# Optimization experiments

Hardware: AMD Instinct MI355X
Metric: run time of the kernel (lower is better)

The kernel has to match this reference:

```python
import jax, jax.numpy as jnp
import numpy as np

B, S, E = 2, 2048, 256
H, D = 8, 32
INF = 2.0 ** 15
EPS = 1e-5


def setup_inputs() -> dict:
    key = jax.random.key(0)
    ks = jax.random.split(key, 10)
    x = jax.random.normal(ks[0], (B, S, E), dtype=jnp.float32)
    mask = jax.random.uniform(ks[1], (B, S), dtype=jnp.float32)
    attn_bias = jax.random.normal(ks[2], (B, H, S, S), dtype=jnp.float32)
    # torch Linear weights have shape (out_dim, in_dim)
    sc = 1.0 / np.sqrt(E)
    Wq = jax.random.normal(ks[3], (H * D, E), dtype=jnp.float32) * sc
    Wk = jax.random.normal(ks[4], (H * D, E), dtype=jnp.float32) * sc
    Wv = jax.random.normal(ks[5], (H * D, E), dtype=jnp.float32) * sc
    # gating init: W=0, b=1 -> perturb slightly so grads are non-trivial
    Wg = jax.random.normal(ks[6], (H * D, E), dtype=jnp.float32) * 0.02
    bg = jnp.ones((H * D,), dtype=jnp.float32)
    # final init: zeros -> perturb slightly
    Wo = jax.random.normal(ks[7], (E, H * D), dtype=jnp.float32) * 0.02
    bo = jnp.zeros((E,), dtype=jnp.float32)
    return {"x": x, "mask": mask, "attn_bias": attn_bias,
            "Wq": Wq, "Wk": Wk, "Wv": Wv, "Wg": Wg, "bg": bg,
            "Wo": Wo, "bo": bo}


def _split_heads(t):
    # [B, S, H*D] -> [B, H, S, D]
    b, s, _ = t.shape
    return t.reshape(b, s, H, D).transpose(0, 2, 1, 3)


def reference(x, mask, attn_bias, Wq, Wk, Wv, Wg, bg, Wo, bo):
    # LayerNorm without affine params
    mu = jnp.mean(x, axis=-1, keepdims=True)
    var = jnp.var(x, axis=-1, keepdims=True)
    xn = (x - mu) * jax.lax.rsqrt(var + EPS)

    scale = 1.0 / jnp.sqrt(jnp.asarray(D, dtype=x.dtype))
    q = _split_heads(xn @ Wq.T) * scale          # [B,H,S,D]
    k = _split_heads(xn @ Wk.T)                   # [B,H,S,D]
    v = _split_heads(xn @ Wv.T)                   # [B,H,S,D]
    gate = jax.nn.sigmoid(_split_heads(xn @ Wg.T + bg))  # [B,H,S,D]

    logits = jnp.einsum('bhic,bhjc->bhij', q, k) + attn_bias  # [B,H,S,S]
    logits = jnp.where(mask[:, None, None, :] < 0.5, -INF, logits)
    attn = jax.nn.softmax(logits, axis=-1)

    out = gate * jnp.einsum('bhij,bhjc->bhic', attn, v)  # [B,H,S,D]
    out = out.transpose(0, 2, 1, 3).reshape(x.shape[0], x.shape[1], H * D)
    return out @ Wo.T + bo
```

## Files before the change

### kernel.cpp

```cpp
#include <hip/hip_runtime.h>
#include <stdint.h>

typedef unsigned short u16;
typedef unsigned int   u32;
typedef __attribute__((ext_vector_type(8))) short    short8;
typedef __attribute__((ext_vector_type(8))) _Float16 half8;
typedef __attribute__((ext_vector_type(4))) _Float16 half4;
typedef __attribute__((ext_vector_type(4))) float    f32x4;

#define BB 2
#define SS 2048
#define EE 256
#define HH 8
#define DDh 32

__device__ __forceinline__ u16 f2b(float f){
  union{u32 u; float f;} c; c.f = f;
  u32 r = c.u + 0x7fffu + ((c.u >> 16) & 1u);
  return (u16)(r >> 16);
}
__device__ __forceinline__ u32 pack2(float lo, float hi){
  return (u32)f2b(lo) | ((u32)f2b(hi) << 16);
}

__device__ __forceinline__ float blockSum(float v, float* red){
  #pragma unroll
  for (int off = 32; off > 0; off >>= 1) v += __shfl_xor(v, off, 64);
  int w = threadIdx.x >> 6;
  if ((threadIdx.x & 63) == 0) red[w] = v;
  __syncthreads();
  float r = (red[0] + red[1]) + (red[2] + red[3]);
  __syncthreads();
  return r;
}

__global__ __launch_bounds__(256) void k_cvt(const float* __restrict__ Wq,
    const float* __restrict__ Wk, const float* __restrict__ Wv,
    const float* __restrict__ Wg, const float* __restrict__ Wo,
    _Float16* __restrict__ wcat, _Float16* __restrict__ woh){
  int id = blockIdx.x * 256 + threadIdx.x;
  int g = id >> 14, idx = id & 16383;
  const float* srcs[5] = {Wq, Wk, Wv, Wg, Wo};
  float4 v = ((const float4*)srcs[g])[idx];
  half4 h = {(_Float16)v.x, (_Float16)v.y, (_Float16)v.z, (_Float16)v.w};
  _Float16* dst = (g < 4) ? (wcat + (size_t)g * 65536) : woh;
  *(half4*)(dst + (size_t)idx * 4) = h;
}

__global__ __launch_bounds__(256) void k_ln(const float* __restrict__ x,
                                            _Float16* __restrict__ xnh){
  __shared__ float red[4];
  int row = blockIdx.x, t = threadIdx.x;
  float xv = x[(size_t)row * EE + t];
  float s  = blockSum(xv, red);
  float ss = blockSum(xv * xv, red);
  float mean = s * (1.0f / EE);
  float var  = ss * (1.0f / EE) - mean * mean;
  float rstd = rsqrtf(var + 1e-5f);
  xnh[(size_t)row * EE + t] = (_Float16)((xv - mean) * rstd);
}

__global__ __launch_bounds__(256) void k_proj(const _Float16* __restrict__ xnh,
    const _Float16* __restrict__ wcat, const float* __restrict__ bg,
    u16* __restrict__ qws, u16* __restrict__ kws,
    u16* __restrict__ vtws, float* __restrict__ gws){
  int t = threadIdx.x, wave = t >> 6, lane = t & 63;
  int q4 = lane >> 4, ln = lane & 15;
  int Mblk = blockIdx.x >> 4, Nblk = blockIdx.x & 15;
  int m0 = Mblk * 64, n0 = Nblk * 64 + wave * 16;
  int n = n0 + ln;
  const _Float16* brow = wcat + (size_t)n * EE;
  f32x4 acc[4];
  #pragma unroll
  for (int mb = 0; mb < 4; ++mb) acc[mb] = (f32x4){0.f,0.f,0.f,0.f};
  for (int k0 = 0; k0 < EE; k0 += 32){
    half8 bf = *(const half8*)(brow + k0 + q4 * 8);
    #pragma unroll
    for (int mb = 0; mb < 4; ++mb){
      half8 af = *(const half8*)(xnh + (size_t)(m0 + mb * 16 + ln) * EE + k0 + q4 * 8);
      acc[mb] = __builtin_amdgcn_mfma_f32_16x16x32_f16(af, bf, acc[mb], 0, 0, 0);
    }
  }
  int mat = n >> 8, c = n & 255;
  int h = c >> 5, d = c & 31;
  int b = m0 >> 11, s0 = (m0 & (SS - 1));
  size_t rowbase = ((size_t)b * HH + h) * SS;
  if (mat == 0){
    #pragma unroll
    for (int mb = 0; mb < 4; ++mb)
      #pragma unroll
      for (int r = 0; r < 4; ++r){
        int s = s0 + mb * 16 + q4 * 4 + r;
        qws[(rowbase + s) * DDh + d] = f2b(acc[mb][r] * 0.17677669529663687f);
      }
  } else if (mat == 1){
    #pragma unroll
    for (int mb = 0; mb < 4; ++mb)
      #pragma unroll
      for (int r = 0; r < 4; ++r){
        int s = s0 + mb * 16 + q4 * 4 + r;
        kws[(rowbase + s) * DDh + d] = f2b(acc[mb][r]);
      }
  } else if (mat == 2){
    u16* vrow = vtws + (((size_t)b * HH + h) * DDh + d) * SS;
    #pragma unroll
    for (int mb = 0; mb < 4; ++mb){
      ushort4 pk;
      pk.x = f2b(acc[mb][0]); pk.y = f2b(acc[mb][1]);
      pk.z = f2b(acc[mb][2]); pk.w = f2b(acc[mb][3]);
      *(ushort4*)(vrow + s0 + mb * 16 + q4 * 4) = pk;
    }
  } else {
    float bgv = bg[c];
    #pragma unroll
    for (int mb = 0; mb < 4; ++mb)
      #pragma unroll
      for (int r = 0; r < 4; ++r){
        int s = s0 + mb * 16 + q4 * 4 + r;
        gws[(rowbase + s) * DDh + d] = 1.0f / (1.0f + __expf(-(acc[mb][r] + bgv)));
      }
  }
}

__global__ __launch_bounds__(256) void k_attn(const u16* __restrict__ qws,
    const u16* __restrict__ kws, const u16* __restrict__ vtws,
    const float* __restrict__ gws, const float* __restrict__ bias,
    const float* __restrict__ mask, _Float16* __restrict__ gouth){
  int t = threadIdx.x;
  int wave = t >> 6, lane = t & 63;
  int q4 = lane >> 4, ln = lane & 15;
  int bh = blockIdx.x >> 5;
  int i0 = (blockIdx.x & 31) * 64 + wave * 16;
  int b = bh >> 3, h = bh & 7;

  short8 qf = *(const short8*)(qws + (((size_t)bh * SS + i0 + ln) * DDh) + q4 * 8);

  const u16*  kb   = kws  + (size_t)bh * SS * DDh;
  const u16*  vt   = vtws + (size_t)bh * DDh * SS;
  const float* br  = bias + ((size_t)bh * SS + i0) * SS;
  const float* mrow= mask + (size_t)b * SS;

  f32x4 O0 = {0.f,0.f,0.f,0.f}, O1 = {0.f,0.f,0.f,0.f};
  float m_run = -INFINITY, l_run = 0.0f;
  const f32x4 zero = {0.f,0.f,0.f,0.f};

  for (int j0 = 0; j0 < SS; j0 += 32){
    short8 ka0 = *(const short8*)(kb + (size_t)(j0 + ln)      * DDh + q4 * 8);
    short8 ka1 = *(const short8*)(kb + (size_t)(j0 + 16 + ln) * DDh + q4 * 8);
    short8 va0 = *(const short8*)(vt + (size_t)ln        * SS + j0 + q4 * 8);
    short8 va1 = *(const short8*)(vt + (size_t)(16 + ln) * SS + j0 + q4 * 8);
    float4 bv0 = *(const float4*)(br + (size_t)ln * SS + j0 + q4 * 4);
    float4 bv1 = *(const float4*)(br + (size_t)ln * SS + j0 + 16 + q4 * 4);
    float4 mv0 = *(const float4*)(mrow + j0 + q4 * 4);
    float4 mv1 = *(const float4*)(mrow + j0 + 16 + q4 * 4);

    f32x4 s0 = __builtin_amdgcn_mfma_f32_16x16x32_bf16(ka0, qf, zero, 0, 0, 0);
    f32x4 s1 = __builtin_amdgcn_mfma_f32_16x16x32_bf16(ka1, qf, zero, 0, 0, 0);

    float lgv[8];
    lgv[0] = (mv0.x >= 0.5f) ? s0[0] + bv0.x : -32768.0f;
    lgv[1] = (mv0.y >= 0.5f) ? s0[1] + bv0.y : -32768.0f;
    lgv[2] = (mv0.z >= 0.5f) ? s0[2] + bv0.z : -32768.0f;
    lgv[3] = (mv0.w >= 0.5f) ? s0[3] + bv0.w : -32768.0f;
    lgv[4] = (mv1.x >= 0.5f) ? s1[0] + bv1.x : -32768.0f;
    lgv[5] = (mv1.y >= 0.5f) ? s1[1] + bv1.y : -32768.0f;
    lgv[6] = (mv1.z >= 0.5f) ? s1[2] + bv1.z : -32768.0f;
    lgv[7] = (mv1.w >= 0.5f) ? s1[3] + bv1.w : -32768.0f;

    float mt = lgv[0];
    #pragma unroll
    for (int r = 1; r < 8; ++r) mt = fmaxf(mt, lgv[r]);
    mt = fmaxf(mt, __shfl_xor(mt, 16, 64));
    mt = fmaxf(mt, __shfl_xor(mt, 32, 64));
    float m_new = fmaxf(m_run, mt);
    float alpha = __expf(m_run - m_new);
    float p[8], ts = 0.0f;
    #pragma unroll
    for (int r = 0; r < 8; ++r){ p[r] = __expf(lgv[r] - m_new); ts += p[r]; }
    ts += __shfl_xor(ts, 16, 64);
    ts += __shfl_xor(ts, 32, 64);
    l_run = l_run * alpha + ts;
    m_run = m_new;
    #pragma unroll
    for (int e = 0; e < 4; ++e){ O0[e] *= alpha; O1[e] *= alpha; }

    u32 P0 = pack2(p[0], p[1]), P1 = pack2(p[2], p[3]);
    u32 P2 = pack2(p[4], p[5]), P3 = pack2(p[6], p[7]);
    int sl  = (q4 & 1) * 32 + ln;
    int sl2 = sl + 16;
    u32 x0 = __shfl((int)P0, sl,  64), x1 = __shfl((int)P1, sl,  64);
    u32 x2 = __shfl((int)P2, sl,  64), x3 = __shfl((int)P3, sl,  64);
    u32 y0 = __shfl((int)P0, sl2, 64), y1 = __shfl((int)P1, sl2, 64);
    u32 y2 = __shfl((int)P2, sl2, 64), y3 = __shfl((int)P3, sl2, 64);
    bool lo = (q4 < 2);
    u32 bb[4];
    bb[0] = lo ? x0 : x2;  bb[1] = lo ? x1 : x3;
    bb[2] = lo ? y0 : y2;  bb[3] = lo ? y1 : y3;
    short8 pf = *(short8*)bb;

    O0 = __builtin_amdgcn_mfma_f32_16x16x32_bf16(va0, pf, O0, 0, 0, 0);
    O1 = __builtin_amdgcn_mfma_f32_16x16x32_bf16(va1, pf, O1, 0, 0, 0);
  }

  float inv = 1.0f / l_run;
  const float* gr = gws + ((size_t)bh * SS + i0 + ln) * DDh;
  float4 g0 = *(const float4*)(gr + q4 * 4);
  float4 g1 = *(const float4*)(gr + 16 + q4 * 4);
  _Float16* orow = gouth + ((size_t)b * SS + (i0 + ln)) * EE + h * DDh;
  half4 w0, w1;
  w0.x = (_Float16)(O0[0] * inv * g0.x);  w0.y = (_Float16)(O0[1] * inv * g0.y);
  w0.z = (_Float16)(O0[2] * inv * g0.z);  w0.w = (_Float16)(O0[3] * inv * g0.w);
  w1.x = (_Float16)(O1[0] * inv * g1.x);  w1.y = (_Float16)(O1[1] * inv * g1.y);
  w1.z = (_Float16)(O1[2] * inv * g1.z);  w1.w = (_Float16)(O1[3] * inv * g1.w);
  *(half4*)(orow + q4 * 4)      = w0;
  *(half4*)(orow + 16 + q4 * 4) = w1;
}

__global__ __launch_bounds__(256) void k_out(const _Float16* __restrict__ gouth,
    const _Float16* __restrict__ woh, const float* __restrict__ bo,
    float* __restrict__ out){
  int t = threadIdx.x, wave = t >> 6, lane = t & 63;
  int q4 = lane >> 4, ln = lane & 15;
  int Mblk = blockIdx.x >> 2, Nblk = blockIdx.x & 3;
  int m0 = Mblk * 64, n0 = Nblk * 64 + wave * 16;
  int n = n0 + ln;
  const _Float16* brow = woh + (size_t)n * EE;
  f32x4 acc[4];
  #pragma unroll
  for (int mb = 0; mb < 4; ++mb) acc[mb] = (f32x4){0.f,0.f,0.f,0.f};
  for (int k0 = 0; k0 < EE; k0 += 32){
    half8 bf = *(const half8*)(brow + k0 + q4 * 8);
    #pragma unroll
    for (int mb = 0; mb < 4; ++mb){
      half8 af = *(const half8*)(gouth + (size_t)(m0 + mb * 16 + ln) * EE + k0 + q4 * 8);
      acc[mb] = __builtin_amdgcn_mfma_f32_16x16x32_f16(af, bf, acc[mb], 0, 0, 0);
    }
  }
  float bov = bo[n];
  #pragma unroll
  for (int mb = 0; mb < 4; ++mb)
    #pragma unroll
    for (int r = 0; r < 4; ++r){
      int m = m0 + mb * 16 + q4 * 4 + r;
      out[(size_t)m * EE + n] = acc[mb][r] + bov;
    }
}

extern "C" void kernel_launch(void* const* d_in, const int* in_sizes, int n_in,
                              void* d_out, int out_size, void* d_ws, size_t ws_size,
                              hipStream_t stream){
  const float* x    = (const float*)d_in[0];
  const float* mask = (const float*)d_in[1];
  const float* bias = (const float*)d_in[2];
  const float* Wq   = (const float*)d_in[3];
  const float* Wk   = (const float*)d_in[4];
  const float* Wv   = (const float*)d_in[5];
  const float* Wg   = (const float*)d_in[6];
  const float* bg   = (const float*)d_in[7];
  const float* Wo   = (const float*)d_in[8];
  const float* bo   = (const float*)d_in[9];
  float* out = (float*)d_out;

  char* ws = (char*)d_ws;
  _Float16* xnh  = (_Float16*)ws;
  u16*  qws  = (u16*) (ws + (2  << 20));
  u16*  kws  = (u16*) (ws + (4  << 20));
  u16*  vtws = (u16*) (ws + (6  << 20));
  float* gws = (float*)(ws + (8  << 20));
  _Float16* gouth = (_Float16*)(ws + (12 << 20));
  _Float16* wcat  = (_Float16*)(ws + (14 << 20));
  _Float16* woh   = (_Float16*)(ws + (15 << 20));

  hipLaunchKernelGGL(k_cvt,  dim3(320),                dim3(256), 0, stream,
                     Wq, Wk, Wv, Wg, Wo, wcat, woh);
  hipLaunchKernelGGL(k_ln,   dim3(BB * SS),            dim3(256), 0, stream, x, xnh);
  hipLaunchKernelGGL(k_proj, dim3(64 * 16),            dim3(256), 0, stream,
                     xnh, wcat, bg, qws, kws, vtws, gws);
  hipLaunchKernelGGL(k_attn, dim3(BB * HH * (SS / 64)), dim3(256), 0, stream,
                     qws, kws, vtws, gws, bias, mask, gouth);
  hipLaunchKernelGGL(k_out,  dim3(64 * 4),             dim3(256), 0, stream,
                     gouth, woh, bo, out);
}
```

Baseline: 435.8 us.

## Double-buffer attention K/V/bias tiles and merge LayerNorm with weight conversion

The attention loop now processes 64-key tiles, with the next tile's K, V and bias loads issued into registers while the current tile computes. This hides global-memory latency on the bias stream, which dominates traffic. It also raises MFMA priority around the PV products and sets launch bounds to two blocks per SM. The LayerNorm and weight-conversion kernels are merged into one launch to save launch overhead. In exchange, register pressure rises, which could cause spills or lower occupancy.

```diff
diff --git a/kernel.cpp b/kernel.cpp
--- a/kernel.cpp
+++ b/kernel.cpp
@@ -34,30 +34,32 @@
   return r;
 }
 
-__global__ __launch_bounds__(256) void k_cvt(const float* __restrict__ Wq,
-    const float* __restrict__ Wk, const float* __restrict__ Wv,
-    const float* __restrict__ Wg, const float* __restrict__ Wo,
+__global__ __launch_bounds__(256) void k_pre(const float* __restrict__ x,
+    _Float16* __restrict__ xnh,
+    const float* __restrict__ Wq, const float* __restrict__ Wk,
+    const float* __restrict__ Wv, const float* __restrict__ Wg,
+    const float* __restrict__ Wo,
     _Float16* __restrict__ wcat, _Float16* __restrict__ woh){
-  int id = blockIdx.x * 256 + threadIdx.x;
-  int g = id >> 14, idx = id & 16383;
-  const float* srcs[5] = {Wq, Wk, Wv, Wg, Wo};
-  float4 v = ((const float4*)srcs[g])[idx];
-  half4 h = {(_Float16)v.x, (_Float16)v.y, (_Float16)v.z, (_Float16)v.w};
-  _Float16* dst = (g < 4) ? (wcat + (size_t)g * 65536) : woh;
-  *(half4*)(dst + (size_t)idx * 4) = h;
-}
-
-__global__ __launch_bounds__(256) void k_ln(const float* __restrict__ x,
-                                            _Float16* __restrict__ xnh){
   __shared__ float red[4];
-  int row = blockIdx.x, t = threadIdx.x;
-  float xv = x[(size_t)row * EE + t];
-  float s  = blockSum(xv, red);
-  float ss = blockSum(xv * xv, red);
-  float mean = s * (1.0f / EE);
-  float var  = ss * (1.0f / EE) - mean * mean;
-  float rstd = rsqrtf(var + 1e-5f);
-  xnh[(size_t)row * EE + t] = (_Float16)((xv - mean) * rstd);
+  int blk = blockIdx.x;
+  if (blk < BB * SS){
+    int t = threadIdx.x;
+    float xv = x[(size_t)blk * EE + t];
+    float s  = blockSum(xv, red);
+    float ss = blockSum(xv * xv, red);
+    float mean = s * (1.0f / EE);
+    float var  = ss * (1.0f / EE) - mean * mean;
+    float rstd = rsqrtf(var + 1e-5f);
+    xnh[(size_t)blk * EE + t] = (_Float16)((xv - mean) * rstd);
+  } else {
+    int id = (blk - BB * SS) * 256 + threadIdx.x;
+    int g = id >> 14, idx = id & 16383;
+    const float* srcs[5] = {Wq, Wk, Wv, Wg, Wo};
+    float4 v = ((const float4*)srcs[g])[idx];
+    half4 h = {(_Float16)v.x, (_Float16)v.y, (_Float16)v.z, (_Float16)v.w};
+    _Float16* dst = (g < 4) ? (wcat + (size_t)g * 65536) : woh;
+    *(half4*)(dst + (size_t)idx * 4) = h;
+  }
 }
 
 __global__ __launch_bounds__(256) void k_proj(const _Float16* __restrict__ xnh,
@@ -122,7 +124,110 @@
   }
 }
 
-__global__ __launch_bounds__(256) void k_attn(const u16* __restrict__ qws,
+struct KTile {
+  short8 ka0, ka1, ka2, ka3;
+  short8 va0, va1, va2, va3;
+  float4 bv0, bv1, bv2, bv3;
+};
+
+__device__ __forceinline__ void tile_load(KTile& T, const u16* __restrict__ kb,
+    const u16* __restrict__ vt, const float* __restrict__ br,
+    int j0, int ln, int q4){
+  T.ka0 = *(const short8*)(kb + (size_t)(j0      + ln) * DDh + q4 * 8);
+  T.ka1 = *(const short8*)(kb + (size_t)(j0 + 16 + ln) * DDh + q4 * 8);
+  T.ka2 = *(const short8*)(kb + (size_t)(j0 + 32 + ln) * DDh + q4 * 8);
+  T.ka3 = *(const short8*)(kb + (size_t)(j0 + 48 + ln) * DDh + q4 * 8);
+  T.va0 = *(const short8*)(vt + (size_t)ln        * SS + j0      + q4 * 8);
+  T.va1 = *(const short8*)(vt + (size_t)ln        * SS + j0 + 32 + q4 * 8);
+  T.va2 = *(const short8*)(vt + (size_t)(16 + ln) * SS + j0      + q4 * 8);
+  T.va3 = *(const short8*)(vt + (size_t)(16 + ln) * SS + j0 + 32 + q4 * 8);
+  const float* b0 = br + (size_t)ln * SS + j0 + q4 * 4;
+  T.bv0 = *(const float4*)(b0);
+  T.bv1 = *(const float4*)(b0 + 16);
+  T.bv2 = *(const float4*)(b0 + 32);
+  T.bv3 = *(const float4*)(b0 + 48);
+}
+
+__device__ __forceinline__ short8 ptrans(const float* p, int sl, int sl2, bool lo){
+  u32 P0 = pack2(p[0], p[1]), P1 = pack2(p[2], p[3]);
+  u32 P2 = pack2(p[4], p[5]), P3 = pack2(p[6], p[7]);
+  u32 x0 = __shfl((int)P0, sl,  64), x1 = __shfl((int)P1, sl,  64);
+  u32 x2 = __shfl((int)P2, sl,  64), x3 = __shfl((int)P3, sl,  64);
+  u32 y0 = __shfl((int)P0, sl2, 64), y1 = __shfl((int)P1, sl2, 64);
+  u32 y2 = __shfl((int)P2, sl2, 64), y3 = __shfl((int)P3, sl2, 64);
+  u32 bb[4];
+  bb[0] = lo ? x0 : x2;  bb[1] = lo ? x1 : x3;
+  bb[2] = lo ? y0 : y2;  bb[3] = lo ? y1 : y3;
+  return *(short8*)bb;
+}
+
+__device__ __forceinline__ void tile_compute(const KTile& T,
+    const float* __restrict__ mrow, int j0, short8 qf,
+    int q4, int sl, int sl2, bool lo,
+    f32x4& O0, f32x4& O1, float& m_run, float& l_run){
+  const f32x4 zero = {0.f,0.f,0.f,0.f};
+  float4 mv0 = *(const float4*)(mrow + j0      + q4 * 4);
+  float4 mv1 = *(const float4*)(mrow + j0 + 16 + q4 * 4);
+  float4 mv2 = *(const float4*)(mrow + j0 + 32 + q4 * 4);
+  float4 mv3 = *(const float4*)(mrow + j0 + 48 + q4 * 4);
+
+  f32x4 s0 = __builtin_amdgcn_mfma_f32_16x16x32_bf16(T.ka0, qf, zero, 0, 0, 0);
+  f32x4 s1 = __builtin_amdgcn_mfma_f32_16x16x32_bf16(T.ka1, qf, zero, 0, 0, 0);
+  f32x4 s2 = __builtin_amdgcn_mfma_f32_16x16x32_bf16(T.ka2, qf, zero, 0, 0, 0);
+  f32x4 s3 = __builtin_amdgcn_mfma_f32_16x16x32_bf16(T.ka3, qf, zero, 0, 0, 0);
+
+  float lg[16];
+  lg[0]  = (mv0.x >= 0.5f) ? s0[0] + T.bv0.x : -32768.0f;
+  lg[1]  = (mv0.y >= 0.5f) ? s0[1] + T.bv0.y : -32768.0f;
+  lg[2]  = (mv0.z >= 0.5f) ? s0[2] + T.bv0.z : -32768.0f;
+  lg[3]  = (mv0.w >= 0.5f) ? s0[3] + T.bv0.w : -32768.0f;
+  lg[4]  = (mv1.x >= 0.5f) ? s1[0] + T.bv1.x : -32768.0f;
+  lg[5]  = (mv1.y >= 0.5f) ? s1[1] + T.bv1.y : -32768.0f;
+  lg[6]  = (mv1.z >= 0.5f) ? s1[2] + T.bv1.z : -32768.0f;
+  lg[7]  = (mv1.w >= 0.5f) ? s1[3] + T.bv1.w : -32768.0f;
+  lg[8]  = (mv2.x >= 0.5f) ? s2[0] + T.bv2.x : -32768.0f;
+  lg[9]  = (mv2.y >= 0.5f) ? s2[1] + T.bv2.y : -32768.0f;
+  lg[10] = (mv2.z >= 0.5f) ? s2[2] + T.bv2.z : -32768.0f;
+  lg[11] = (mv2.w >= 0.5f) ? s2[3] + T.bv2.w : -32768.0f;
+  lg[12] = (mv3.x >= 0.5f) ? s3[0] + T.bv3.x : -32768.0f;
+  lg[13] = (mv3.y >= 0.5f) ? s3[1] + T.bv3.y : -32768.0f;
+  lg[14] = (mv3.z >= 0.5f) ? s3[2] + T.bv3.z : -32768.0f;
+  lg[15] = (mv3.w >= 0.5f) ? s3[3] + T.bv3.w : -32768.0f;
+
+  float ma = fmaxf(fmaxf(lg[0], lg[1]),  fmaxf(lg[2],  lg[3]));
+  float mb = fmaxf(fmaxf(lg[4], lg[5]),  fmaxf(lg[6],  lg[7]));
+  float mc = fmaxf(fmaxf(lg[8], lg[9]),  fmaxf(lg[10], lg[11]));
+  float md = fmaxf(fmaxf(lg[12],lg[13]), fmaxf(lg[14], lg[15]));
+  float mt = fmaxf(fmaxf(ma, mb), fmaxf(mc, md));
+  mt = fmaxf(mt, __shfl_xor(mt, 16, 64));
+  mt = fmaxf(mt, __shfl_xor(mt, 32, 64));
+  float m_new = fmaxf(m_run, mt);
+  float alpha = __expf(m_run - m_new);
+
+  float p[16];
+  #pragma unroll
+  for (int r = 0; r < 16; ++r) p[r] = __expf(lg[r] - m_new);
+  float ts = (((p[0]+p[1])+(p[2]+p[3])) + ((p[4]+p[5])+(p[6]+p[7])))
+           + (((p[8]+p[9])+(p[10]+p[11])) + ((p[12]+p[13])+(p[14]+p[15])));
+  ts += __shfl_xor(ts, 16, 64);
+  ts += __shfl_xor(ts, 32, 64);
+  l_run = l_run * alpha + ts;
+  m_run = m_new;
+  #pragma unroll
+  for (int e = 0; e < 4; ++e){ O0[e] *= alpha; O1[e] *= alpha; }
+
+  short8 pfA = ptrans(p,     sl, sl2, lo);
+  short8 pfB = ptrans(p + 8, sl, sl2, lo);
+
+  __builtin_amdgcn_s_setprio(1);
+  O0 = __builtin_amdgcn_mfma_f32_16x16x32_bf16(T.va0, pfA, O0, 0, 0, 0);
+  O0 = __builtin_amdgcn_mfma_f32_16x16x32_bf16(T.va1, pfB, O0, 0, 0, 0);
+  O1 = __builtin_amdgcn_mfma_f32_16x16x32_bf16(T.va2, pfA, O1, 0, 0, 0);
+  O1 = __builtin_amdgcn_mfma_f32_16x16x32_bf16(T.va3, pfB, O1, 0, 0, 0);
+  __builtin_amdgcn_s_setprio(0);
+}
+
+__global__ __launch_bounds__(256, 2) void k_attn(const u16* __restrict__ qws,
     const u16* __restrict__ kws, const u16* __restrict__ vtws,
     const float* __restrict__ gws, const float* __restrict__ bias,
     const float* __restrict__ mask, _Float16* __restrict__ gouth){
@@ -132,9 +237,11 @@
   int bh = blockIdx.x >> 5;
   int i0 = (blockIdx.x & 31) * 64 + wave * 16;
   int b = bh >> 3, h = bh & 7;
+  int sl  = (q4 & 1) * 32 + ln;
+  int sl2 = sl + 16;
+  bool lo = (q4 < 2);
 
   short8 qf = *(const short8*)(qws + (((size_t)bh * SS + i0 + ln) * DDh) + q4 * 8);
-
   const u16*  kb   = kws  + (size_t)bh * SS * DDh;
   const u16*  vt   = vtws + (size_t)bh * DDh * SS;
   const float* br  = bias + ((size_t)bh * SS + i0) * SS;
@@ -142,64 +249,15 @@
 
   f32x4 O0 = {0.f,0.f,0.f,0.f}, O1 = {0.f,0.f,0.f,0.f};
   float m_run = -INFINITY, l_run = 0.0f;
-  const f32x4 zero = {0.f,0.f,0.f,0.f};
-
-  for (int j0 = 0; j0 < SS; j0 += 32){
-    short8 ka0 = *(const short8*)(kb + (size_t)(j0 + ln)      * DDh + q4 * 8);
-    short8 ka1 = *(const short8*)(kb + (size_t)(j0 + 16 + ln) * DDh + q4 * 8);
-    short8 va0 = *(const short8*)(vt + (size_t)ln        * SS + j0 + q4 * 8);
-    short8 va1 = *(const short8*)(vt + (size_t)(16 + ln) * SS + j0 + q4 * 8);
-    float4 bv0 = *(const float4*)(br + (size_t)ln * SS + j0 + q4 * 4);
-    float4 bv1 = *(const float4*)(br + (size_t)ln * SS + j0 + 16 + q4 * 4);
-    float4 mv0 = *(const float4*)(mrow + j0 + q4 * 4);
-    float4 mv1 = *(const float4*)(mrow + j0 + 16 + q4 * 4);
-
-    f32x4 s0 = __builtin_amdgcn_mfma_f32_16x16x32_bf16(ka0, qf, zero, 0, 0, 0);
-    f32x4 s1 = __builtin_amdgcn_mfma_f32_16x16x32_bf16(ka1, qf, zero, 0, 0, 0);
-
-    float lgv[8];
-    lgv[0] = (mv0.x >= 0.5f) ? s0[0] + bv0.x : -32768.0f;
-    lgv[1] = (mv0.y >= 0.5f) ? s0[1] + bv0.y : -32768.0f;
-    lgv[2] = (mv0.z >= 0.5f) ? s0[2] + bv0.z : -32768.0f;
-    lgv[3] = (mv0.w >= 0.5f) ? s0[3] + bv0.w : -32768.0f;
-    lgv[4] = (mv1.x >= 0.5f) ? s1[0] + bv1.x : -32768.0f;
-    lgv[5] = (mv1.y >= 0.5f) ? s1[1] + bv1.y : -32768.0f;
-    lgv[6] = (mv1.z >= 0.5f) ? s1[2] + bv1.z : -32768.0f;
-    lgv[7] = (mv1.w >= 0.5f) ? s1[3] + bv1.w : -32768.0f;
-
-    float mt = lgv[0];
-    #pragma unroll
-    for (int r = 1; r < 8; ++r) mt = fmaxf(mt, lgv[r]);
-    mt = fmaxf(mt, __shfl_xor(mt, 16, 64));
-    mt = fmaxf(mt, __shfl_xor(mt, 32, 64));
-    float m_new = fmaxf(m_run, mt);
-    float alpha = __expf(m_run - m_new);
-    float p[8], ts = 0.0f;
-    #pragma unroll
-    for (int r = 0; r < 8; ++r){ p[r] = __expf(lgv[r] - m_new); ts += p[r]; }
-    ts += __shfl_xor(ts, 16, 64);
-    ts += __shfl_xor(ts, 32, 64);
-    l_run = l_run * alpha + ts;
-    m_run = m_new;
-    #pragma unroll
-    for (int e = 0; e < 4; ++e){ O0[e] *= alpha; O1[e] *= alpha; }
-
-    u32 P0 = pack2(p[0], p[1]), P1 = pack2(p[2], p[3]);
-    u32 P2 = pack2(p[4], p[5]), P3 = pack2(p[6], p[7]);
-    int sl  = (q4 & 1) * 32 + ln;
-    int sl2 = sl + 16;
-    u32 x0 = __shfl((int)P0, sl,  64), x1 = __shfl((int)P1, sl,  64);
-    u32 x2 = __shfl((int)P2, sl,  64), x3 = __shfl((int)P3, sl,  64);
-    u32 y0 = __shfl((int)P0, sl2, 64), y1 = __shfl((int)P1, sl2, 64);
-    u32 y2 = __shfl((int)P2, sl2, 64), y3 = __shfl((int)P3, sl2, 64);
-    bool lo = (q4 < 2);
-    u32 bb[4];
-    bb[0] = lo ? x0 : x2;  bb[1] = lo ? x1 : x3;
-    bb[2] = lo ? y0 : y2;  bb[3] = lo ? y1 : y3;
-    short8 pf = *(short8*)bb;
-
-    O0 = __builtin_amdgcn_mfma_f32_16x16x32_bf16(va0, pf, O0, 0, 0, 0);
-    O1 = __builtin_amdgcn_mfma_f32_16x16x32_bf16(va1, pf, O1, 0, 0, 0);
+
+  KTile A, Bt;
+  tile_load(A, kb, vt, br, 0, ln, q4);
+  for (int j0 = 0; j0 < SS; j0 += 128){
+    tile_load(Bt, kb, vt, br, j0 + 64, ln, q4);
+    tile_compute(A, mrow, j0, qf, q4, sl, sl2, lo, O0, O1, m_run, l_run);
+    if (j0 + 128 < SS)
+      tile_load(A, kb, vt, br, j0 + 128, ln, q4);
+    tile_compute(Bt, mrow, j0 + 64, qf, q4, sl, sl2, lo, O0, O1, m_run, l_run);
   }
 
   float inv = 1.0f / l_run;
@@ -271,9 +329,8 @@
   _Float16* wcat  = (_Float16*)(ws + (14 << 20));
   _Float16* woh   = (_Float16*)(ws + (15 << 20));
 
-  hipLaunchKernelGGL(k_cvt,  dim3(320),                dim3(256), 0, stream,
-                     Wq, Wk, Wv, Wg, Wo, wcat, woh);
-  hipLaunchKernelGGL(k_ln,   dim3(BB * SS),            dim3(256), 0, stream, x, xnh);
+  hipLaunchKernelGGL(k_pre,  dim3(BB * SS + 320),      dim3(256), 0, stream,
+                     x, xnh, Wq, Wk, Wv, Wg, Wo, wcat, woh);
   hipLaunchKernelGGL(k_proj, dim3(64 * 16),            dim3(256), 0, stream,
                      xnh, wcat, bg, qws, kws, vtws, gws);
   hipLaunchKernelGGL(k_attn, dim3(BB * HH * (SS / 64)), dim3(256), 0, stream,
```

Result: no change. 435.7 us (-0.0%).
